# Optimization experiments

Hardware: AMD Instinct MI355X
Metric: run time of the kernel (lower is better)

Reference implementation:

```python
import jax, jax.numpy as jnp
import numpy as np

D_MODEL = 768
NUM_HEADS = 12
D_K = D_MODEL // NUM_HEADS


def setup_inputs() -> dict:
    key = jax.random.key(0)
    ks = jax.random.split(key, 11)
    B, L = 1, 4096
    s = 1.0 / np.sqrt(D_MODEL)
    return {
        "q": jax.random.normal(ks[0], (B, L, D_MODEL), jnp.float32),
        "k": jax.random.normal(ks[1], (B, L, D_MODEL), jnp.float32),
        "v": jax.random.normal(ks[2], (B, L, D_MODEL), jnp.float32),
        "Wq": jax.random.normal(ks[3], (D_MODEL, D_MODEL), jnp.float32) * s,
        "bq": jax.random.normal(ks[4], (D_MODEL,), jnp.float32) * s,
        "Wk": jax.random.normal(ks[5], (D_MODEL, D_MODEL), jnp.float32) * s,
        "bk": jax.random.normal(ks[6], (D_MODEL,), jnp.float32) * s,
        "Wv": jax.random.normal(ks[7], (D_MODEL, D_MODEL), jnp.float32) * s,
        "bv": jax.random.normal(ks[8], (D_MODEL,), jnp.float32) * s,
        "Wo": jax.random.normal(ks[9], (D_MODEL, D_MODEL), jnp.float32) * s,
        "bo": jax.random.normal(ks[10], (D_MODEL,), jnp.float32) * s,
    }


def reference(q, k, v, Wq, bq, Wk, bk, Wv, bv, Wo, bo):
    B, L, _ = q.shape
    # linear projections (torch Linear: x @ W.T + b)
    qp = q @ Wq.T + bq
    kp = k @ Wk.T + bk
    vp = v @ Wv.T + bv
    # split heads: (B, H, L, d_k)
    def split(x):
        return x.reshape(B, L, NUM_HEADS, D_K).transpose(0, 2, 1, 3)
    qh, kh, vh = split(qp), split(kp), split(vp)
    scale = 1.0 / jnp.sqrt(jnp.asarray(D_K, qh.dtype))
    scores = jnp.einsum("bhqd,bhkd->bhqk", qh, kh) * scale  # (B,H,L,L)
    weights = jax.nn.softmax(scores, axis=-1)
    out = jnp.einsum("bhqk,bhkd->bhqd", weights, vh)
    out = out.transpose(0, 2, 1, 3).reshape(B, L, D_MODEL)
    return out @ Wo.T + bo
```

## Files before the change

kernel.cpp:

```cpp
#include <hip/hip_runtime.h>
#include <stdint.h>
#include <math.h>

#define L_SEQ  4096
#define DMODEL 768
#define NHEADS 12
#define DKH    64
#define QSCALE 0.18033688011112042f

typedef _Float16 f16;
typedef __attribute__((ext_vector_type(8))) _Float16 half8;
typedef __attribute__((ext_vector_type(4))) _Float16 half4;
typedef __attribute__((ext_vector_type(4))) float f32x4;
typedef __attribute__((ext_vector_type(16))) float f32x16;
typedef __attribute__((ext_vector_type(4))) unsigned int uint4v;

#define MFMA16(a, b, c) __builtin_amdgcn_mfma_f32_16x16x32_f16(a, b, c, 0, 0, 0)
#define MFMA32(a, b, c) __builtin_amdgcn_mfma_f32_32x32x16_f16(a, b, c, 0, 0, 0)

#define NE ((size_t)L_SEQ * DMODEL)
#define WE ((size_t)DMODEL * DMODEL)

static __device__ __forceinline__ unsigned int pack2(float a, float b) {
  return __builtin_bit_cast(unsigned int, __builtin_amdgcn_cvt_pkrtz(a, b));
}

__global__ __launch_bounds__(256)
void cvt_all(const float* __restrict__ q, const float* __restrict__ k,
             const float* __restrict__ v, const float* __restrict__ Wq,
             const float* __restrict__ Wk, const float* __restrict__ Wv,
             const float* __restrict__ Wo, f16* __restrict__ x16,
             f16* __restrict__ w16)
{
  const size_t NE4 = NE / 4, WE4 = WE / 4;
  size_t i = (size_t)blockIdx.x * 256 + threadIdx.x;
  const float* srcs[7] = {q, k, v, Wq, Wk, Wv, Wo};
  f16* dsts[7] = {x16, x16 + NE, x16 + 2 * NE,
                  w16, w16 + WE, w16 + 2 * WE, w16 + 3 * WE};
  const size_t sz4[7] = {NE4, NE4, NE4, WE4, WE4, WE4, WE4};
  int r = 0; size_t off = i;
  while (off >= sz4[r]) { off -= sz4[r]; ++r; }
  float4 f = reinterpret_cast<const float4*>(srcs[r])[off];
  half4 h; h[0] = (f16)f.x; h[1] = (f16)f.y; h[2] = (f16)f.z; h[3] = (f16)f.w;
  reinterpret_cast<half4*>(dsts[r])[off] = h;
}

__global__ __launch_bounds__(256)
void qkv_gemm(const f16* __restrict__ x16, const f16* __restrict__ w16,
              const float* __restrict__ bq, const float* __restrict__ bk,
              const float* __restrict__ bv,
              f16* __restrict__ Qp, f16* __restrict__ Kp, f16* __restrict__ VpT)
{
  __shared__ f16 As[128][72];
  __shared__ f16 Bs[64][72];
  const int tid  = threadIdx.x;
  const int lane = tid & 63, wid = tid >> 6;
  const int lq   = lane & 15, quad = lane >> 4;
  const int wm   = (wid & 1) * 64, wn = (wid >> 1) * 32;
  const int m0   = blockIdx.y * 128;
  const int widx = blockIdx.x / 12;
  const int n0   = (blockIdx.x % 12) * 64;
  const f16* X = x16 + (size_t)widx * NE;
  const f16* W = w16 + (size_t)widx * WE;
  const float* Bv = (widx == 0) ? bq : (widx == 1) ? bk : bv;

  const int arow = tid >> 1, aseg = (tid & 1) * 32;
  const int brow = tid >> 2, bseg = (tid & 3) * 16;
  const f16* aptr = X + (size_t)(m0 + arow) * DMODEL + aseg;
  const f16* bptr = W + (size_t)(n0 + brow) * DMODEL + bseg;

  half8 a0 = *reinterpret_cast<const half8*>(aptr);
  half8 a1 = *reinterpret_cast<const half8*>(aptr + 8);
  half8 a2 = *reinterpret_cast<const half8*>(aptr + 16);
  half8 a3 = *reinterpret_cast<const half8*>(aptr + 24);
  half8 b0 = *reinterpret_cast<const half8*>(bptr);
  half8 b1 = *reinterpret_cast<const half8*>(bptr + 8);

  f32x4 acc[4][2] = {};

  for (int k0 = 0; k0 < DMODEL; k0 += 64) {
    *reinterpret_cast<half8*>(&As[arow][aseg])      = a0;
    *reinterpret_cast<half8*>(&As[arow][aseg + 8])  = a1;
    *reinterpret_cast<half8*>(&As[arow][aseg + 16]) = a2;
    *reinterpret_cast<half8*>(&As[arow][aseg + 24]) = a3;
    *reinterpret_cast<half8*>(&Bs[brow][bseg])      = b0;
    *reinterpret_cast<half8*>(&Bs[brow][bseg + 8])  = b1;
    __syncthreads();

    if (k0 + 64 < DMODEL) {
      a0 = *reinterpret_cast<const half8*>(aptr + k0 + 64);
      a1 = *reinterpret_cast<const half8*>(aptr + k0 + 72);
      a2 = *reinterpret_cast<const half8*>(aptr + k0 + 80);
      a3 = *reinterpret_cast<const half8*>(aptr + k0 + 88);
      b0 = *reinterpret_cast<const half8*>(bptr + k0 + 64);
      b1 = *reinterpret_cast<const half8*>(bptr + k0 + 72);
    }

#pragma unroll
    for (int ks = 0; ks < 2; ++ks) {
      half8 bf[2];
#pragma unroll
      for (int nf = 0; nf < 2; ++nf)
        bf[nf] = *reinterpret_cast<half8*>(&Bs[wn + nf * 16 + lq][ks * 32 + quad * 8]);
#pragma unroll
      for (int mf = 0; mf < 4; ++mf) {
        half8 af = *reinterpret_cast<half8*>(&As[wm + mf * 16 + lq][ks * 32 + quad * 8]);
#pragma unroll
        for (int nf = 0; nf < 2; ++nf)
          acc[mf][nf] = MFMA16(af, bf[nf], acc[mf][nf]);
      }
    }
    __syncthreads();
  }

#pragma unroll
  for (int nf = 0; nf < 2; ++nf) {
    const int col  = n0 + wn + nf * 16 + lq;
    const float bias = Bv[col];
#pragma unroll
    for (int mf = 0; mf < 4; ++mf) {
      const int rowb = m0 + wm + mf * 16 + quad * 4;
      if (widx == 2) {
        half4 o4;
#pragma unroll
        for (int r = 0; r < 4; ++r) o4[r] = (f16)(acc[mf][nf][r] + bias);
        *reinterpret_cast<half4*>(VpT + (size_t)col * L_SEQ + rowb) = o4;
      } else if (widx == 0) {
#pragma unroll
        for (int r = 0; r < 4; ++r)
          Qp[(size_t)(rowb + r) * DMODEL + col] = (f16)((acc[mf][nf][r] + bias) * QSCALE);
      } else {
#pragma unroll
        for (int r = 0; r < 4; ++r)
          Kp[(size_t)(rowb + r) * DMODEL + col] = (f16)(acc[mf][nf][r] + bias);
      }
    }
  }
}

__global__ __launch_bounds__(256, 3)
void attn_mfma4(const f16* __restrict__ Qp, const f16* __restrict__ Kp,
                const f16* __restrict__ VpT, f16* __restrict__ AO)
{
  const int h  = blockIdx.x;
  const int q0 = blockIdx.y * 64;
  const int tid  = threadIdx.x;
  const int lane = tid & 63, wid = tid >> 6;
  const int l31  = lane & 31, hc = lane >> 5;
  const int qh   = wid & 1, kh = wid >> 1;

  __shared__ __align__(16) char smem[36864];
  f16 (*Ks)[64][72] = (f16 (*)[64][72])smem;
  f16 (*Vt)[64][72] = (f16 (*)[64][72])(smem + 18432);
  float* Of  = (float*)smem;
  float* lf  = (float*)(smem + 16384);
  f16*   Of16 = (f16*)(smem + 16640);

  half8 qf[4];
#pragma unroll
  for (int st = 0; st < 4; ++st)
    qf[st] = *reinterpret_cast<const half8*>(
        Qp + (size_t)(q0 + qh * 32 + l31) * DMODEL + h * DKH + st * 16 + hc * 8);

  f32x16 oacc[2] = {};
  float lsum = 0.0f;

  const int srow = tid >> 2, sseg = (tid & 3) * 16;
  const f16* kbase = Kp  + (size_t)srow * DMODEL + h * DKH + sseg;
  const f16* vbase = VpT + (size_t)(h * DKH + srow) * L_SEQ + sseg;

  half8 k0 = *reinterpret_cast<const half8*>(kbase);
  half8 k1 = *reinterpret_cast<const half8*>(kbase + 8);
  half8 v0 = *reinterpret_cast<const half8*>(vbase);
  half8 v1 = *reinterpret_cast<const half8*>(vbase + 8);

  int p = 0;
  for (int kt = 0; kt < L_SEQ; kt += 64) {
    *reinterpret_cast<half8*>(&Ks[p][srow][sseg])     = k0;
    *reinterpret_cast<half8*>(&Ks[p][srow][sseg + 8]) = k1;
    *reinterpret_cast<half8*>(&Vt[p][srow][sseg])     = v0;
    *reinterpret_cast<half8*>(&Vt[p][srow][sseg + 8]) = v1;
    __syncthreads();

    if (kt + 64 < L_SEQ) {
      const f16* kn = kbase + (size_t)(kt + 64) * DMODEL;
      const f16* vn = vbase + (kt + 64);
      k0 = *reinterpret_cast<const half8*>(kn);
      k1 = *reinterpret_cast<const half8*>(kn + 8);
      v0 = *reinterpret_cast<const half8*>(vn);
      v1 = *reinterpret_cast<const half8*>(vn + 8);
    }

    __builtin_amdgcn_s_setprio(1);

    f32x16 s = {};
#pragma unroll
    for (int st = 0; st < 4; ++st) {
      half8 kf = *reinterpret_cast<half8*>(&Ks[p][kh * 32 + l31][st * 16 + hc * 8]);
      s = MFMA32(kf, qf[st], s);
    }

    unsigned int pk[8];
#pragma unroll
    for (int i = 0; i < 8; ++i) {
      float p0 = __builtin_amdgcn_exp2f(s[2 * i]);
      float p1 = __builtin_amdgcn_exp2f(s[2 * i + 1]);
      lsum += p0 + p1;
      pk[i] = pack2(p0, p1);
    }

#pragma unroll
    for (int st = 0; st < 2; ++st) {
      unsigned int w0 = pk[4 * st + 0], w1 = pk[4 * st + 1];
      unsigned int w2 = pk[4 * st + 2], w3 = pk[4 * st + 3];
      asm("v_permlane32_swap_b32 %0, %1" : "+v"(w0), "+v"(w2));
      asm("v_permlane32_swap_b32 %0, %1" : "+v"(w1), "+v"(w3));
      uint4v pw; pw[0] = w0; pw[1] = w1; pw[2] = w2; pw[3] = w3;
      half8 pf = __builtin_bit_cast(half8, pw);
#pragma unroll
      for (int a = 0; a < 2; ++a) {
        half8 vf = *reinterpret_cast<half8*>(&Vt[p][a * 32 + l31][kh * 32 + st * 16 + hc * 8]);
        oacc[a] = MFMA32(vf, pf, oacc[a]);
      }
    }
    __builtin_amdgcn_s_setprio(0);
    p ^= 1;
  }
  __syncthreads();

  float lw = lsum + __shfl_xor(lsum, 32);

  if (kh == 0) {
#pragma unroll
    for (int a = 0; a < 2; ++a)
#pragma unroll
      for (int r = 0; r < 16; ++r) {
        int d = a * 32 + (r & 3) + 8 * (r >> 2) + 4 * hc;
        Of[((qh * 64) + d) * 32 + l31] = oacc[a][r];
      }
    if (lane < 32) lf[qh * 32 + l31] = lw;
  }
  __syncthreads();
  if (kh == 1) {
    const float inv = 1.0f / (lf[qh * 32 + l31] + lw);
#pragma unroll
    for (int a = 0; a < 2; ++a)
#pragma unroll
      for (int r = 0; r < 16; ++r) {
        int d = a * 32 + (r & 3) + 8 * (r >> 2) + 4 * hc;
        float val = (Of[((qh * 64) + d) * 32 + l31] + oacc[a][r]) * inv;
        Of16[(qh * 32 + l31) * 64 + d] = (f16)val;
      }
  }
  __syncthreads();

  *reinterpret_cast<half8*>(AO + (size_t)(q0 + srow) * DMODEL + h * DKH + sseg) =
      *reinterpret_cast<half8*>(&Of16[srow * 64 + sseg]);
  *reinterpret_cast<half8*>(AO + (size_t)(q0 + srow) * DMODEL + h * DKH + sseg + 8) =
      *reinterpret_cast<half8*>(&Of16[srow * 64 + sseg + 8]);
}

__global__ __launch_bounds__(256)
void out_gemm(const f16* __restrict__ A, const f16* __restrict__ W,
              const float* __restrict__ Bv, float* __restrict__ O)
{
  __shared__ f16 As[64][72];
  __shared__ f16 Bs[64][72];
  const int tid  = threadIdx.x;
  const int lane = tid & 63, wid = tid >> 6;
  const int lq   = lane & 15, quad = lane >> 4;
  const int wm   = (wid & 1) * 32, wn = (wid >> 1) * 32;
  const int m0   = blockIdx.y * 64, n0 = blockIdx.x * 64;

  const int row = tid >> 2, seg = (tid & 3) * 16;
  const f16* aptr = A + (size_t)(m0 + row) * DMODEL + seg;
  const f16* bptr = W + (size_t)(n0 + row) * DMODEL + seg;

  half8 a0 = *reinterpret_cast<const half8*>(aptr);
  half8 a1 = *reinterpret_cast<const half8*>(aptr + 8);
  half8 b0 = *reinterpret_cast<const half8*>(bptr);
  half8 b1 = *reinterpret_cast<const half8*>(bptr + 8);

  f32x4 acc[2][2] = {};

  for (int k0 = 0; k0 < DMODEL; k0 += 64) {
    *reinterpret_cast<half8*>(&As[row][seg])     = a0;
    *reinterpret_cast<half8*>(&As[row][seg + 8]) = a1;
    *reinterpret_cast<half8*>(&Bs[row][seg])     = b0;
    *reinterpret_cast<half8*>(&Bs[row][seg + 8]) = b1;
    __syncthreads();

    if (k0 + 64 < DMODEL) {
      a0 = *reinterpret_cast<const half8*>(aptr + k0 + 64);
      a1 = *reinterpret_cast<const half8*>(aptr + k0 + 72);
      b0 = *reinterpret_cast<const half8*>(bptr + k0 + 64);
      b1 = *reinterpret_cast<const half8*>(bptr + k0 + 72);
    }

#pragma unroll
    for (int ks = 0; ks < 2; ++ks) {
      half8 bf[2];
#pragma unroll
      for (int nf = 0; nf < 2; ++nf)
        bf[nf] = *reinterpret_cast<half8*>(&Bs[wn + nf * 16 + lq][ks * 32 + quad * 8]);
#pragma unroll
      for (int mf = 0; mf < 2; ++mf) {
        half8 af = *reinterpret_cast<half8*>(&As[wm + mf * 16 + lq][ks * 32 + quad * 8]);
#pragma unroll
        for (int nf = 0; nf < 2; ++nf)
          acc[mf][nf] = MFMA16(af, bf[nf], acc[mf][nf]);
      }
    }
    __syncthreads();
  }

#pragma unroll
  for (int nf = 0; nf < 2; ++nf) {
    const int col = n0 + wn + nf * 16 + lq;
    const float bias = Bv[col];
#pragma unroll
    for (int mf = 0; mf < 2; ++mf) {
      const int rowb = m0 + wm + mf * 16 + quad * 4;
#pragma unroll
      for (int r = 0; r < 4; ++r)
        O[(size_t)(rowb + r) * DMODEL + col] = acc[mf][nf][r] + bias;
    }
  }
}

extern "C" void kernel_launch(void* const* d_in, const int* in_sizes, int n_in,
                              void* d_out, int out_size, void* d_ws, size_t ws_size,
                              hipStream_t stream) {
  const float* q  = (const float*)d_in[0];
  const float* k  = (const float*)d_in[1];
  const float* v  = (const float*)d_in[2];
  const float* Wq = (const float*)d_in[3];
  const float* bq = (const float*)d_in[4];
  const float* Wk = (const float*)d_in[5];
  const float* bk = (const float*)d_in[6];
  const float* Wv = (const float*)d_in[7];
  const float* bv = (const float*)d_in[8];
  const float* Wo = (const float*)d_in[9];
  const float* bo = (const float*)d_in[10];
  float* out = (float*)d_out;

  f16* x16 = (f16*)d_ws;
  f16* w16 = x16 + 3 * NE;
  f16* Qp  = w16 + 4 * WE;
  f16* Kp  = Qp + NE;
  f16* VpT = Kp + NE;
  f16* AO  = VpT + NE;

  const int ncvt = (int)((3 * (NE / 4) + 4 * (WE / 4)) / 256);
  cvt_all<<<ncvt, 256, 0, stream>>>(q, k, v, Wq, Wk, Wv, Wo, x16, w16);

  dim3 gqkv(36, L_SEQ / 128);
  qkv_gemm<<<gqkv, 256, 0, stream>>>(x16, w16, bq, bk, bv, Qp, Kp, VpT);

  dim3 gattn(NHEADS, L_SEQ / 64);
  attn_mfma4<<<gattn, 256, 0, stream>>>(Qp, Kp, VpT, AO);

  dim3 gout(DMODEL / 64, L_SEQ / 64);
  out_gemm<<<gout, 256, 0, stream>>>(AO, w16 + 3 * WE, bo, out);
}
```

Measured before the change: 226.0 us.

## Fuse activation fp16 conversion into QKV GEMM and restructure attention loop

Drops the separate fp32-to-fp16 conversion of q/k/v: the QKV GEMM now loads fp32 activations directly and converts them while staging into shared memory, so only the weights go through a conversion kernel. In attention, the K/V shared-memory store is moved one iteration ahead (prefetch two tiles deep) and the loop is unrolled by two. The softmax row sum is now computed with an extra MFMA against a ones vector instead of scalar adds and a cross-lane shuffle. Costs are double the register footprint for fp32 A prefetch, an extra MFMA per step, and higher register pressure from unrolling.

Measured after the change: 250.6 us. 10.9% more time.

```diff
diff --git a/kernel.cpp b/kernel.cpp
--- a/kernel.cpp
+++ b/kernel.cpp
@@ -12,6 +12,7 @@
 typedef __attribute__((ext_vector_type(8))) _Float16 half8;
 typedef __attribute__((ext_vector_type(4))) _Float16 half4;
 typedef __attribute__((ext_vector_type(4))) float f32x4;
+typedef __attribute__((ext_vector_type(4))) float fv4;
 typedef __attribute__((ext_vector_type(16))) float f32x16;
 typedef __attribute__((ext_vector_type(4))) unsigned int uint4v;
 
@@ -26,27 +27,23 @@
 }
 
 __global__ __launch_bounds__(256)
-void cvt_all(const float* __restrict__ q, const float* __restrict__ k,
-             const float* __restrict__ v, const float* __restrict__ Wq,
-             const float* __restrict__ Wk, const float* __restrict__ Wv,
-             const float* __restrict__ Wo, f16* __restrict__ x16,
-             f16* __restrict__ w16)
+void cvt_w(const float* __restrict__ Wq, const float* __restrict__ Wk,
+           const float* __restrict__ Wv, const float* __restrict__ Wo,
+           f16* __restrict__ w16)
 {
-  const size_t NE4 = NE / 4, WE4 = WE / 4;
+  const size_t WE4 = WE / 4;
   size_t i = (size_t)blockIdx.x * 256 + threadIdx.x;
-  const float* srcs[7] = {q, k, v, Wq, Wk, Wv, Wo};
-  f16* dsts[7] = {x16, x16 + NE, x16 + 2 * NE,
-                  w16, w16 + WE, w16 + 2 * WE, w16 + 3 * WE};
-  const size_t sz4[7] = {NE4, NE4, NE4, WE4, WE4, WE4, WE4};
-  int r = 0; size_t off = i;
-  while (off >= sz4[r]) { off -= sz4[r]; ++r; }
+  const float* srcs[4] = {Wq, Wk, Wv, Wo};
+  int r = (int)(i / WE4);
+  size_t off = i - (size_t)r * WE4;
   float4 f = reinterpret_cast<const float4*>(srcs[r])[off];
   half4 h; h[0] = (f16)f.x; h[1] = (f16)f.y; h[2] = (f16)f.z; h[3] = (f16)f.w;
-  reinterpret_cast<half4*>(dsts[r])[off] = h;
+  reinterpret_cast<half4*>(w16 + (size_t)r * WE)[off] = h;
 }
 
 __global__ __launch_bounds__(256)
-void qkv_gemm(const f16* __restrict__ x16, const f16* __restrict__ w16,
+void qkv_gemm(const float* __restrict__ xq, const float* __restrict__ xk,
+              const float* __restrict__ xv, const f16* __restrict__ w16,
               const float* __restrict__ bq, const float* __restrict__ bk,
               const float* __restrict__ bv,
               f16* __restrict__ Qp, f16* __restrict__ Kp, f16* __restrict__ VpT)
@@ -60,38 +57,42 @@
   const int m0   = blockIdx.y * 128;
   const int widx = blockIdx.x / 12;
   const int n0   = (blockIdx.x % 12) * 64;
-  const f16* X = x16 + (size_t)widx * NE;
+  const float* X = (widx == 0) ? xq : (widx == 1) ? xk : xv;
   const f16* W = w16 + (size_t)widx * WE;
   const float* Bv = (widx == 0) ? bq : (widx == 1) ? bk : bv;
 
   const int arow = tid >> 1, aseg = (tid & 1) * 32;
   const int brow = tid >> 2, bseg = (tid & 3) * 16;
-  const f16* aptr = X + (size_t)(m0 + arow) * DMODEL + aseg;
-  const f16* bptr = W + (size_t)(n0 + brow) * DMODEL + bseg;
-
-  half8 a0 = *reinterpret_cast<const half8*>(aptr);
-  half8 a1 = *reinterpret_cast<const half8*>(aptr + 8);
-  half8 a2 = *reinterpret_cast<const half8*>(aptr + 16);
-  half8 a3 = *reinterpret_cast<const half8*>(aptr + 24);
+  const float* aptr = X + (size_t)(m0 + arow) * DMODEL + aseg;
+  const f16*   bptr = W + (size_t)(n0 + brow) * DMODEL + bseg;
+
+  fv4 a4[8];
+#pragma unroll
+  for (int u = 0; u < 8; ++u) a4[u] = reinterpret_cast<const fv4*>(aptr)[u];
   half8 b0 = *reinterpret_cast<const half8*>(bptr);
   half8 b1 = *reinterpret_cast<const half8*>(bptr + 8);
 
   f32x4 acc[4][2] = {};
 
   for (int k0 = 0; k0 < DMODEL; k0 += 64) {
-    *reinterpret_cast<half8*>(&As[arow][aseg])      = a0;
-    *reinterpret_cast<half8*>(&As[arow][aseg + 8])  = a1;
-    *reinterpret_cast<half8*>(&As[arow][aseg + 16]) = a2;
-    *reinterpret_cast<half8*>(&As[arow][aseg + 24]) = a3;
-    *reinterpret_cast<half8*>(&Bs[brow][bseg])      = b0;
-    *reinterpret_cast<half8*>(&Bs[brow][bseg + 8])  = b1;
+#pragma unroll
+    for (int u = 0; u < 4; ++u) {
+      half8 h;
+#pragma unroll
+      for (int e = 0; e < 4; ++e) {
+        h[e]     = (f16)a4[2 * u][e];
+        h[4 + e] = (f16)a4[2 * u + 1][e];
+      }
+      *reinterpret_cast<half8*>(&As[arow][aseg + u * 8]) = h;
+    }
+    *reinterpret_cast<half8*>(&Bs[brow][bseg])     = b0;
+    *reinterpret_cast<half8*>(&Bs[brow][bseg + 8]) = b1;
     __syncthreads();
 
     if (k0 + 64 < DMODEL) {
-      a0 = *reinterpret_cast<const half8*>(aptr + k0 + 64);
-      a1 = *reinterpret_cast<const half8*>(aptr + k0 + 72);
-      a2 = *reinterpret_cast<const half8*>(aptr + k0 + 80);
-      a3 = *reinterpret_cast<const half8*>(aptr + k0 + 88);
+#pragma unroll
+      for (int u = 0; u < 8; ++u)
+        a4[u] = reinterpret_cast<const fv4*>(aptr + k0 + 64)[u];
       b0 = *reinterpret_cast<const half8*>(bptr + k0 + 64);
       b1 = *reinterpret_cast<const half8*>(bptr + k0 + 72);
     }
@@ -162,8 +163,13 @@
     qf[st] = *reinterpret_cast<const half8*>(
         Qp + (size_t)(q0 + qh * 32 + l31) * DMODEL + h * DKH + st * 16 + hc * 8);
 
+  half8 ones;
+#pragma unroll
+  for (int e = 0; e < 8; ++e) ones[e] = (f16)1.0f;
+  const f32x16 zf = {};
+
   f32x16 oacc[2] = {};
-  float lsum = 0.0f;
+  f32x16 lacc = {};
 
   const int srow = tid >> 2, sseg = (tid & 3) * 16;
   const f16* kbase = Kp  + (size_t)srow * DMODEL + h * DKH + sseg;
@@ -173,18 +179,29 @@
   half8 k1 = *reinterpret_cast<const half8*>(kbase + 8);
   half8 v0 = *reinterpret_cast<const half8*>(vbase);
   half8 v1 = *reinterpret_cast<const half8*>(vbase + 8);
+  *reinterpret_cast<half8*>(&Ks[0][srow][sseg])     = k0;
+  *reinterpret_cast<half8*>(&Ks[0][srow][sseg + 8]) = k1;
+  *reinterpret_cast<half8*>(&Vt[0][srow][sseg])     = v0;
+  *reinterpret_cast<half8*>(&Vt[0][srow][sseg + 8]) = v1;
+  k0 = *reinterpret_cast<const half8*>(kbase + (size_t)64 * DMODEL);
+  k1 = *reinterpret_cast<const half8*>(kbase + (size_t)64 * DMODEL + 8);
+  v0 = *reinterpret_cast<const half8*>(vbase + 64);
+  v1 = *reinterpret_cast<const half8*>(vbase + 64 + 8);
 
   int p = 0;
+#pragma unroll 2
   for (int kt = 0; kt < L_SEQ; kt += 64) {
-    *reinterpret_cast<half8*>(&Ks[p][srow][sseg])     = k0;
-    *reinterpret_cast<half8*>(&Ks[p][srow][sseg + 8]) = k1;
-    *reinterpret_cast<half8*>(&Vt[p][srow][sseg])     = v0;
-    *reinterpret_cast<half8*>(&Vt[p][srow][sseg + 8]) = v1;
     __syncthreads();
 
     if (kt + 64 < L_SEQ) {
-      const f16* kn = kbase + (size_t)(kt + 64) * DMODEL;
-      const f16* vn = vbase + (kt + 64);
+      *reinterpret_cast<half8*>(&Ks[p ^ 1][srow][sseg])     = k0;
+      *reinterpret_cast<half8*>(&Ks[p ^ 1][srow][sseg + 8]) = k1;
+      *reinterpret_cast<half8*>(&Vt[p ^ 1][srow][sseg])     = v0;
+      *reinterpret_cast<half8*>(&Vt[p ^ 1][srow][sseg + 8]) = v1;
+    }
+    if (kt + 128 < L_SEQ) {
+      const f16* kn = kbase + (size_t)(kt + 128) * DMODEL;
+      const f16* vn = vbase + (kt + 128);
       k0 = *reinterpret_cast<const half8*>(kn);
       k1 = *reinterpret_cast<const half8*>(kn + 8);
       v0 = *reinterpret_cast<const half8*>(vn);
@@ -193,9 +210,10 @@
 
     __builtin_amdgcn_s_setprio(1);
 
-    f32x16 s = {};
-#pragma unroll
-    for (int st = 0; st < 4; ++st) {
+    half8 kf0 = *reinterpret_cast<half8*>(&Ks[p][kh * 32 + l31][hc * 8]);
+    f32x16 s = MFMA32(kf0, qf[0], zf);
+#pragma unroll
+    for (int st = 1; st < 4; ++st) {
       half8 kf = *reinterpret_cast<half8*>(&Ks[p][kh * 32 + l31][st * 16 + hc * 8]);
       s = MFMA32(kf, qf[st], s);
     }
@@ -205,7 +223,6 @@
     for (int i = 0; i < 8; ++i) {
       float p0 = __builtin_amdgcn_exp2f(s[2 * i]);
       float p1 = __builtin_amdgcn_exp2f(s[2 * i + 1]);
-      lsum += p0 + p1;
       pk[i] = pack2(p0, p1);
     }
 
@@ -217,6 +234,7 @@
       asm("v_permlane32_swap_b32 %0, %1" : "+v"(w1), "+v"(w3));
       uint4v pw; pw[0] = w0; pw[1] = w1; pw[2] = w2; pw[3] = w3;
       half8 pf = __builtin_bit_cast(half8, pw);
+      lacc = MFMA32(ones, pf, lacc);
 #pragma unroll
       for (int a = 0; a < 2; ++a) {
         half8 vf = *reinterpret_cast<half8*>(&Vt[p][a * 32 + l31][kh * 32 + st * 16 + hc * 8]);
@@ -228,7 +246,7 @@
   }
   __syncthreads();
 
-  float lw = lsum + __shfl_xor(lsum, 32);
+  const float lw = lacc[0];
 
   if (kh == 0) {
 #pragma unroll
@@ -344,18 +362,17 @@
   const float* bo = (const float*)d_in[10];
   float* out = (float*)d_out;
 
-  f16* x16 = (f16*)d_ws;
-  f16* w16 = x16 + 3 * NE;
+  f16* w16 = (f16*)d_ws;
   f16* Qp  = w16 + 4 * WE;
   f16* Kp  = Qp + NE;
   f16* VpT = Kp + NE;
   f16* AO  = VpT + NE;
 
-  const int ncvt = (int)((3 * (NE / 4) + 4 * (WE / 4)) / 256);
-  cvt_all<<<ncvt, 256, 0, stream>>>(q, k, v, Wq, Wk, Wv, Wo, x16, w16);
+  const int ncvt = (int)(WE / 256);
+  cvt_w<<<ncvt, 256, 0, stream>>>(Wq, Wk, Wv, Wo, w16);
 
   dim3 gqkv(36, L_SEQ / 128);
-  qkv_gemm<<<gqkv, 256, 0, stream>>>(x16, w16, bq, bk, bv, Qp, Kp, VpT);
+  qkv_gemm<<<gqkv, 256, 0, stream>>>(q, k, v, w16, bq, bk, bv, Qp, Kp, VpT);
 
   dim3 gattn(NHEADS, L_SEQ / 64);
   attn_mfma4<<<gattn, 256, 0, stream>>>(Qp, Kp, VpT, AO);
```
